# Kernel tuning notes

Measured on AMD Instinct MI355X. Metric: run time of the kernel, lower is better.

Reference implementation:

```python
import jax, jax.numpy as jnp
import numpy as np

N = 32768      # nodes
E = 262144     # edges (avg degree 8)
D = 128        # d_model (= per-head out_channels, concat=False)
H = 4          # heads
C = D          # out_channels per head
R = 64         # rel_dim (edge_dim)
NREL = 64      # n_rels
L = 2          # num_layers
LEAK = 0.2     # GATv2 leaky_relu slope
LN_EPS = 1e-5


def setup_inputs() -> dict:
    key = jax.random.key(0)
    ks = jax.random.split(key, 12)
    sdD = 1.0 / np.sqrt(D)
    sdR = 1.0 / np.sqrt(R)
    return {
        "x_flat": jax.random.normal(ks[0], (N, D), jnp.float32),
        "edge_index": jax.random.randint(ks[1], (2, E), 0, N, jnp.int64),
        "edge_type": jax.random.randint(ks[2], (E,), 0, NREL, jnp.int64),
        "valid_mask_flat": jnp.ones((N,), bool),
        "rel_emb": jax.random.normal(ks[3], (NREL, R), jnp.float32) * 0.1,
        "Wl": jax.random.normal(ks[4], (L, D, H * C), jnp.float32) * sdD,
        "bl": jnp.zeros((L, H * C), jnp.float32),
        "Wr": jax.random.normal(ks[5], (L, D, H * C), jnp.float32) * sdD,
        "br": jnp.zeros((L, H * C), jnp.float32),
        "We": jax.random.normal(ks[6], (L, R, H * C), jnp.float32) * sdR,
        "att": jax.random.normal(ks[7], (L, H, C), jnp.float32) * 0.1,
        "bias_o": jnp.zeros((L, D), jnp.float32),
        "ln_g": jnp.ones((L, D), jnp.float32),
        "ln_b": jnp.zeros((L, D), jnp.float32),
    }


def _gatv2_layer(h, src, dst, ea, Wl, bl, Wr, br, We, att, b):
    # h: [N,D]; src/dst: [E+N]; ea: [E+N,R] edge embeddings (incl. self loops)
    xl = (h @ Wl + bl).reshape(N, H, C)   # source transform
    xr = (h @ Wr + br).reshape(N, H, C)   # target transform
    ep = (ea @ We).reshape(-1, H, C)
    e = jax.nn.leaky_relu(xl[src] + xr[dst] + ep, LEAK)   # [E+N,H,C]
    logits = jnp.einsum('ehc,hc->eh', e, att)             # [E+N,H]
    # segment softmax over destination node
    m = jax.ops.segment_max(logits, dst, num_segments=N)
    m = jnp.where(jnp.isfinite(m), m, 0.0)
    p = jnp.exp(logits - m[dst])
    denom = jax.ops.segment_sum(p, dst, num_segments=N)
    alpha = p / (denom[dst] + 1e-16)                      # [E+N,H]
    out = jax.ops.segment_sum(alpha[:, :, None] * xl[src], dst, num_segments=N)
    return out.mean(axis=1) + b                           # concat=False -> head mean


def reference(x_flat, edge_index, edge_type, valid_mask_flat,
              rel_emb, Wl, bl, Wr, br, We, att, bias_o, ln_g, ln_b):
    x = jnp.where(valid_mask_flat[:, None], x_flat, 0.0)
    src, dst = edge_index[0], edge_index[1]
    ea = rel_emb[edge_type]                               # [E,R]
    # PyG add_self_loops with fill_value='mean': self-loop edge_attr is the
    # mean of incoming edge attrs per target node (0 if no incoming edges).
    ones = jnp.ones((E,), x.dtype)
    deg = jax.ops.segment_sum(ones, dst, num_segments=N)
    self_attr = jax.ops.segment_sum(ea, dst, num_segments=N) / jnp.maximum(deg, 1.0)[:, None]
    loop = jnp.arange(N, dtype=src.dtype)
    src_f = jnp.concatenate([src, loop])
    dst_f = jnp.concatenate([dst, loop])
    ea_f = jnp.concatenate([ea, self_attr], axis=0)

    h = x
    for l in range(L):
        msg = _gatv2_layer(h, src_f, dst_f, ea_f,
                           Wl[l], bl[l], Wr[l], br[l], We[l], att[l], bias_o[l])
        msg = jax.nn.gelu(msg, approximate=False)         # dropout = identity (eval)
        hn = h + msg
        mu = jnp.mean(hn, axis=-1, keepdims=True)
        var = jnp.mean(jnp.square(hn - mu), axis=-1, keepdims=True)
        h = (hn - mu) / jnp.sqrt(var + LN_EPS) * ln_g[l] + ln_b[l]
    return jnp.where(valid_mask_flat[:, None], h, 0.0)
```

## Files before the change

### kernel.cpp

```cpp
#include <hip/hip_runtime.h>
#include <hip/hip_bf16.h>
#include <math.h>

#define NN 32768
#define EE 262144
#define DM 128
#define HH 4
#define CC 128
#define HC 512
#define RD 64
#define NRELS 64
#define LEAKS 0.2f
#define LNEPS 1e-5f

typedef __hip_bfloat16 bf16;
typedef __attribute__((ext_vector_type(8))) short short8;
typedef __attribute__((ext_vector_type(4))) float f32x4;

__device__ __forceinline__ void unpack8(uint4 u, float* f) {
    f[0] = __uint_as_float((u.x & 0xffffu) << 16);
    f[1] = __uint_as_float(u.x & 0xffff0000u);
    f[2] = __uint_as_float((u.y & 0xffffu) << 16);
    f[3] = __uint_as_float(u.y & 0xffff0000u);
    f[4] = __uint_as_float((u.z & 0xffffu) << 16);
    f[5] = __uint_as_float(u.z & 0xffff0000u);
    f[6] = __uint_as_float((u.w & 0xffffu) << 16);
    f[7] = __uint_as_float(u.w & 0xffff0000u);
}

__global__ void k_deg(const int* __restrict__ dst, int* __restrict__ deg) {
    int e = blockIdx.x * 256 + threadIdx.x;
    if (e < EE) atomicAdd(&deg[dst[e]], 1);
}

__global__ void k_scan1(const int* __restrict__ deg, int* __restrict__ rowptr,
                        int* __restrict__ bsum) {
    __shared__ int s[256];
    int b = blockIdx.x, t = threadIdx.x;
    int v = deg[b * 256 + t];
    s[t] = v;
    __syncthreads();
    for (int off = 1; off < 256; off <<= 1) {
        int x = (t >= off) ? s[t - off] : 0;
        __syncthreads();
        s[t] += x;
        __syncthreads();
    }
    rowptr[b * 256 + t] = s[t] - v;
    if (t == 255) bsum[b] = s[255];
}

__global__ void k_scan2(const int* __restrict__ bsum, int* __restrict__ boff) {
    __shared__ int s[128];
    int t = threadIdx.x;
    int v = bsum[t];
    s[t] = v;
    __syncthreads();
    for (int off = 1; off < 128; off <<= 1) {
        int x = (t >= off) ? s[t - off] : 0;
        __syncthreads();
        s[t] += x;
        __syncthreads();
    }
    boff[t] = s[t] - v;
    if (t == 127) boff[128] = s[127];
}

__global__ void k_scan3(int* __restrict__ rowptr, const int* __restrict__ boff) {
    int i = blockIdx.x * 256 + threadIdx.x;
    rowptr[i] += boff[i >> 8];
    if (i == NN - 1) rowptr[NN] = boff[128];
}

__global__ void k_fill(const int* __restrict__ src, const int* __restrict__ dst,
                       const int* __restrict__ etype, const int* __restrict__ rowptr,
                       int* __restrict__ cursor, unsigned* __restrict__ csr) {
    int e = blockIdx.x * 256 + threadIdx.x;
    if (e < EE) {
        int d = dst[e];
        int pos = atomicAdd(&cursor[d], 1);
        csr[rowptr[d] + pos] = (unsigned)src[e] | ((unsigned)etype[e] << 16);
    }
}

__global__ void k_cast(const float* __restrict__ x, bf16* __restrict__ hb) {
    int i = blockIdx.x * 256 + threadIdx.x;
    const float4* p = (const float4*)x;
    float4 f0 = p[i * 2], f1 = p[i * 2 + 1];
    bf16 o[8];
    o[0] = __float2bfloat16(f0.x); o[1] = __float2bfloat16(f0.y);
    o[2] = __float2bfloat16(f0.z); o[3] = __float2bfloat16(f0.w);
    o[4] = __float2bfloat16(f1.x); o[5] = __float2bfloat16(f1.y);
    o[6] = __float2bfloat16(f1.z); o[7] = __float2bfloat16(f1.w);
    *reinterpret_cast<uint4*>(hb + (size_t)i * 8) = *reinterpret_cast<uint4*>(o);
}

__global__ void k_repack2(const float* __restrict__ Wl, const float* __restrict__ Wr,
                          bf16* __restrict__ Wt) {
    int idx = blockIdx.x * 256 + threadIdx.x;
    int l = idx >> 17;
    int rem = idx & 131071;
    int k = rem >> 10;
    int c = rem & 1023;
    const float* WlL = Wl + (size_t)l * DM * HC;
    const float* WrL = Wr + (size_t)l * DM * HC;
    float v = (c < HC) ? WlL[k * HC + c] : WrL[k * HC + (c - HC)];
    Wt[(size_t)l * 1024 * DM + (size_t)c * DM + k] = __float2bfloat16(v);
}

__global__ void k_wep2(const float* __restrict__ rel_emb, const float* __restrict__ We,
                       bf16* __restrict__ wep) {
    int l = blockIdx.x >> 6;
    int r = blockIdx.x & 63;
    int c = threadIdx.x;
    const float* WeL = We + (size_t)l * RD * HC;
    __shared__ float a[RD];
    if (c < RD) a[c] = rel_emb[r * RD + c];
    __syncthreads();
    float s = 0.f;
#pragma unroll 8
    for (int k = 0; k < RD; ++k) s += a[k] * WeL[k * HC + c];
    wep[(size_t)l * NRELS * HC + (size_t)r * HC + c] = __float2bfloat16(s);
}

__global__ __launch_bounds__(256) void k_gemm_mfma(
    const bf16* __restrict__ hb, const bf16* __restrict__ Wt,
    const float* __restrict__ bl, const float* __restrict__ br,
    bf16* __restrict__ xlb, bf16* __restrict__ xrb) {
    int lane = threadIdx.x & 63;
    int wave = threadIdx.x >> 6;
    int rbase = blockIdx.x * 32;
    int cbase = blockIdx.y * 256 + wave * 64;
    int lr = lane & 15;
    int lk = lane >> 4;
    const short* ha = (const short*)hb;
    const short* wa = (const short*)Wt;

    short8 a[2][4], b[4][4];
#pragma unroll
    for (int mi = 0; mi < 2; ++mi)
#pragma unroll
        for (int kk = 0; kk < 4; ++kk)
            a[mi][kk] = *(const short8*)(ha + (size_t)(rbase + mi * 16 + lr) * DM + kk * 32 + lk * 8);
#pragma unroll
    for (int ni = 0; ni < 4; ++ni)
#pragma unroll
        for (int kk = 0; kk < 4; ++kk)
            b[ni][kk] = *(const short8*)(wa + (size_t)(cbase + ni * 16 + lr) * DM + kk * 32 + lk * 8);

    f32x4 c[2][4];
#pragma unroll
    for (int mi = 0; mi < 2; ++mi)
#pragma unroll
        for (int ni = 0; ni < 4; ++ni)
            c[mi][ni] = (f32x4){0.f, 0.f, 0.f, 0.f};

#pragma unroll
    for (int kk = 0; kk < 4; ++kk)
#pragma unroll
        for (int mi = 0; mi < 2; ++mi)
#pragma unroll
            for (int ni = 0; ni < 4; ++ni)
                c[mi][ni] = __builtin_amdgcn_mfma_f32_16x16x32_bf16(
                    a[mi][kk], b[ni][kk], c[mi][ni], 0, 0, 0);

#pragma unroll
    for (int ni = 0; ni < 4; ++ni) {
        int col = cbase + ni * 16 + lr;
        float bv = (col < HC) ? bl[col] : br[col - HC];
        bf16* outp;
        int cc;
        if (col < HC) { outp = xlb; cc = col; } else { outp = xrb; cc = col - HC; }
#pragma unroll
        for (int mi = 0; mi < 2; ++mi) {
#pragma unroll
            for (int r = 0; r < 4; ++r) {
                int row = rbase + mi * 16 + lk * 4 + r;
                outp[(size_t)row * HC + cc] = __float2bfloat16(c[mi][ni][r] + bv);
            }
        }
    }
}

__global__ __launch_bounds__(1024, 8) void k_node(
    const bf16* __restrict__ xlb, const bf16* __restrict__ xrb,
    const bf16* __restrict__ wep,
    const unsigned* __restrict__ csr, const int* __restrict__ rowptr,
    const float* __restrict__ attL, const float* __restrict__ biasL,
    const float* __restrict__ lngL, const float* __restrict__ lnbL,
    const float* __restrict__ h_in, float* __restrict__ h_out,
    bf16* __restrict__ hb_out) {
    __shared__ short wepS[NRELS * HC];
    int tid = threadIdx.x;
    {
        const uint4* ws = (const uint4*)wep;
        uint4* wd = (uint4*)wepS;
#pragma unroll
        for (int i = 0; i < 4; ++i) wd[tid + i * 1024] = ws[tid + i * 1024];
    }
    __syncthreads();

    int lane = tid & 63;
    int wave = tid >> 6;
    int n = blockIdx.x * 16 + wave;
    int head = lane >> 4;
    const int g0 = lane * 8;
    const int ch0 = (lane & 15) * 8;
    const short* xla = (const short*)xlb;

    float attv[8];
#pragma unroll
    for (int j = 0; j < 8; ++j) attv[j] = attL[head * CC + ch0 + j];

    float xrn[8], xln[8];
    unpack8(*(const uint4*)((const short*)xrb + (size_t)n * HC + g0), xrn);
    unpack8(*(const uint4*)(xla + (size_t)n * HC + g0), xln);

    float m = -1e30f;
    float denom = 0.f;
    float acc[8], wpsum[8];
#pragma unroll
    for (int j = 0; j < 8; ++j) { acc[j] = 0.f; wpsum[j] = 0.f; }

    int r0 = rowptr[n], r1 = rowptr[n + 1];
    int d = r1 - r0;
    if (d > 0) {
        unsigned u = csr[r0];
        uint4 xv = *(const uint4*)(xla + (size_t)(u & 0xffffu) * HC + g0);
        for (int i = r0; i < r1; ++i) {
            int inx = (i + 1 < r1) ? (i + 1) : i;
            unsigned un = csr[inx];
            uint4 xn = *(const uint4*)(xla + (size_t)(un & 0xffffu) * HC + g0);
            uint4 wv = *(const uint4*)(wepS + (u >> 16) * HC + g0);
            float xs[8], wp[8];
            unpack8(xv, xs);
            unpack8(wv, wp);
            float p2 = 0.f;
#pragma unroll
            for (int j = 0; j < 8; ++j) {
                wpsum[j] += wp[j];
                float v = xs[j] + xrn[j] + wp[j];
                v = (v > 0.f) ? v : LEAKS * v;
                p2 += v * attv[j];
            }
            p2 += __shfl_xor(p2, 1);
            p2 += __shfl_xor(p2, 2);
            p2 += __shfl_xor(p2, 4);
            p2 += __shfl_xor(p2, 8);
            float mnew = fmaxf(m, p2);
            float scale = __expf(m - mnew);
            float p = __expf(p2 - mnew);
            denom = denom * scale + p;
#pragma unroll
            for (int j = 0; j < 8; ++j) acc[j] = acc[j] * scale + p * xs[j];
            m = mnew;
            u = un;
            xv = xn;
        }
    }

    float invd = (d > 0) ? (1.0f / (float)d) : 1.0f;
    float p2 = 0.f;
#pragma unroll
    for (int j = 0; j < 8; ++j) {
        float v = xln[j] + xrn[j] + wpsum[j] * invd;
        v = (v > 0.f) ? v : LEAKS * v;
        p2 += v * attv[j];
    }
    p2 += __shfl_xor(p2, 1);
    p2 += __shfl_xor(p2, 2);
    p2 += __shfl_xor(p2, 4);
    p2 += __shfl_xor(p2, 8);
    {
        float mnew = fmaxf(m, p2);
        float scale = __expf(m - mnew);
        float p = __expf(p2 - mnew);
        denom = denom * scale + p;
#pragma unroll
        for (int j = 0; j < 8; ++j) acc[j] = acc[j] * scale + p * xln[j];
    }

    float inv = 1.0f / (denom + 1e-16f);
    const float4* hp = (const float4*)(h_in + (size_t)n * DM + ch0);
    float4 h0 = hp[0], h1 = hp[1];
    float hin[8] = {h0.x, h0.y, h0.z, h0.w, h1.x, h1.y, h1.z, h1.w};
    float hn[8];
    float lsum = 0.f, lsq = 0.f;
#pragma unroll
    for (int j = 0; j < 8; ++j) {
        float v = acc[j] * inv;
        v += __shfl_xor(v, 16);
        v += __shfl_xor(v, 32);
        float x = v * 0.25f + biasL[ch0 + j];
        float ge = 0.5f * x * (1.0f + erff(x * 0.70710678f));
        float hv = hin[j] + ge;
        hn[j] = hv;
        lsum += hv;
        lsq += hv * hv;
    }
    lsum += __shfl_xor(lsum, 1);
    lsum += __shfl_xor(lsum, 2);
    lsum += __shfl_xor(lsum, 4);
    lsum += __shfl_xor(lsum, 8);
    lsq += __shfl_xor(lsq, 1);
    lsq += __shfl_xor(lsq, 2);
    lsq += __shfl_xor(lsq, 4);
    lsq += __shfl_xor(lsq, 8);
    float mu = lsum * (1.0f / 128.f);
    float var = lsq * (1.0f / 128.f) - mu * mu;
    float rstd = rsqrtf(var + LNEPS);
    if (lane < 16) {
#pragma unroll
        for (int j = 0; j < 8; ++j) {
            float o = (hn[j] - mu) * rstd * lngL[ch0 + j] + lnbL[ch0 + j];
            h_out[(size_t)n * DM + ch0 + j] = o;
            hb_out[(size_t)n * DM + ch0 + j] = __float2bfloat16(o);
        }
    }
}

extern "C" void kernel_launch(void* const* d_in, const int* in_sizes, int n_in,
                              void* d_out, int out_size, void* d_ws, size_t ws_size,
                              hipStream_t stream) {
    const float* x_flat   = (const float*)d_in[0];
    const int*   edge_idx = (const int*)d_in[1];
    const int*   edge_typ = (const int*)d_in[2];
    const float* rel_emb  = (const float*)d_in[4];
    const float* Wl       = (const float*)d_in[5];
    const float* bl       = (const float*)d_in[6];
    const float* Wr       = (const float*)d_in[7];
    const float* br       = (const float*)d_in[8];
    const float* We       = (const float*)d_in[9];
    const float* att      = (const float*)d_in[10];
    const float* bias_o   = (const float*)d_in[11];
    const float* ln_g     = (const float*)d_in[12];
    const float* ln_b     = (const float*)d_in[13];

    const int* srcp = edge_idx;
    const int* dstp = edge_idx + EE;

    char* w = (char*)d_ws;
    auto alloc = [&](size_t bytes) -> void* {
        void* p = (void*)w;
        w += (bytes + 255) & ~(size_t)255;
        return p;
    };
    bf16*  xlb    = (bf16*)alloc((size_t)NN * HC * 2);
    bf16*  xrb    = (bf16*)alloc((size_t)NN * HC * 2);
    bf16*  hb     = (bf16*)alloc((size_t)NN * DM * 2);
    float* h_mid  = (float*)alloc((size_t)NN * DM * 4);
    bf16*  wep    = (bf16*)alloc((size_t)2 * NRELS * HC * 2);
    bf16*  Wt     = (bf16*)alloc((size_t)2 * 1024 * DM * 2);
    int*   deg    = (int*)alloc((size_t)NN * 4);
    int*   rowptr = (int*)alloc((size_t)(NN + 1) * 4);
    int*   cursor = (int*)alloc((size_t)NN * 4);
    int*   bsum   = (int*)alloc((size_t)128 * 4);
    int*   boff   = (int*)alloc((size_t)129 * 4);
    unsigned* csr = (unsigned*)alloc((size_t)EE * 4);

    hipMemsetAsync(deg, 0, (size_t)NN * 4, stream);
    hipMemsetAsync(cursor, 0, (size_t)NN * 4, stream);

    k_deg<<<EE / 256, 256, 0, stream>>>(dstp, deg);
    k_scan1<<<NN / 256, 256, 0, stream>>>(deg, rowptr, bsum);
    k_scan2<<<1, 128, 0, stream>>>(bsum, boff);
    k_scan3<<<NN / 256, 256, 0, stream>>>(rowptr, boff);
    k_fill<<<EE / 256, 256, 0, stream>>>(srcp, dstp, edge_typ, rowptr, cursor, csr);
    k_cast<<<NN * DM / 8 / 256, 256, 0, stream>>>(x_flat, hb);
    k_wep2<<<128, 512, 0, stream>>>(rel_emb, We, wep);
    k_repack2<<<1024, 256, 0, stream>>>(Wl, Wr, Wt);

    const float* h = x_flat;
    for (int l = 0; l < 2; ++l) {
        k_gemm_mfma<<<dim3(NN / 32, 4), 256, 0, stream>>>(
            hb, Wt + (size_t)l * 1024 * DM,
            bl + (size_t)l * HC, br + (size_t)l * HC, xlb, xrb);
        float* hout = (l == 0) ? h_mid : (float*)d_out;
        k_node<<<NN / 16, 1024, 0, stream>>>(xlb, xrb, wep + (size_t)l * NRELS * HC,
                                             csr, rowptr,
                                             att + (size_t)l * HH * CC,
                                             bias_o + (size_t)l * DM,
                                             ln_g + (size_t)l * DM,
                                             ln_b + (size_t)l * DM,
                                             h, hout, hb);
        h = hout;
    }
}
```

Baseline: 462.1 us.

## Pair-unroll node aggregation, drop LDS staging, merge prep kernels

The node kernel now works through edges two at a time with prefetch of the next pair. It reads relation projections straight from global/L2 instead of staging 64KB into LDS per block, and it uses 256-thread blocks. The online softmax skips the rescale when no lane's max increases. Separately, the cast, repack and rel-projection kernels are merged into one launch, the two memsets are combined, edge kernels use 1024-thread blocks, and the final layer no longer writes an unused bf16 copy. The aim is to cut LDS fill overhead, launch count and latency-bound edge loop stalls, with the risk of more global gather traffic for the wep rows.

```diff
diff --git a/kernel.cpp b/kernel.cpp
--- a/kernel.cpp
+++ b/kernel.cpp
@@ -29,8 +29,8 @@
 }
 
 __global__ void k_deg(const int* __restrict__ dst, int* __restrict__ deg) {
-    int e = blockIdx.x * 256 + threadIdx.x;
-    if (e < EE) atomicAdd(&deg[dst[e]], 1);
+    int e = blockIdx.x * 1024 + threadIdx.x;
+    atomicAdd(&deg[dst[e]], 1);
 }
 
 __global__ void k_scan1(const int* __restrict__ deg, int* __restrict__ rowptr,
@@ -75,52 +75,52 @@
 __global__ void k_fill(const int* __restrict__ src, const int* __restrict__ dst,
                        const int* __restrict__ etype, const int* __restrict__ rowptr,
                        int* __restrict__ cursor, unsigned* __restrict__ csr) {
-    int e = blockIdx.x * 256 + threadIdx.x;
-    if (e < EE) {
-        int d = dst[e];
-        int pos = atomicAdd(&cursor[d], 1);
-        csr[rowptr[d] + pos] = (unsigned)src[e] | ((unsigned)etype[e] << 16);
-    }
-}
-
-__global__ void k_cast(const float* __restrict__ x, bf16* __restrict__ hb) {
-    int i = blockIdx.x * 256 + threadIdx.x;
-    const float4* p = (const float4*)x;
-    float4 f0 = p[i * 2], f1 = p[i * 2 + 1];
-    bf16 o[8];
-    o[0] = __float2bfloat16(f0.x); o[1] = __float2bfloat16(f0.y);
-    o[2] = __float2bfloat16(f0.z); o[3] = __float2bfloat16(f0.w);
-    o[4] = __float2bfloat16(f1.x); o[5] = __float2bfloat16(f1.y);
-    o[6] = __float2bfloat16(f1.z); o[7] = __float2bfloat16(f1.w);
-    *reinterpret_cast<uint4*>(hb + (size_t)i * 8) = *reinterpret_cast<uint4*>(o);
-}
-
-__global__ void k_repack2(const float* __restrict__ Wl, const float* __restrict__ Wr,
-                          bf16* __restrict__ Wt) {
-    int idx = blockIdx.x * 256 + threadIdx.x;
-    int l = idx >> 17;
-    int rem = idx & 131071;
-    int k = rem >> 10;
-    int c = rem & 1023;
-    const float* WlL = Wl + (size_t)l * DM * HC;
-    const float* WrL = Wr + (size_t)l * DM * HC;
-    float v = (c < HC) ? WlL[k * HC + c] : WrL[k * HC + (c - HC)];
-    Wt[(size_t)l * 1024 * DM + (size_t)c * DM + k] = __float2bfloat16(v);
-}
-
-__global__ void k_wep2(const float* __restrict__ rel_emb, const float* __restrict__ We,
+    int e = blockIdx.x * 1024 + threadIdx.x;
+    int d = dst[e];
+    int pos = atomicAdd(&cursor[d], 1);
+    csr[rowptr[d] + pos] = (unsigned)src[e] | ((unsigned)etype[e] << 16);
+}
+
+__global__ void k_prep(const float* __restrict__ x, bf16* __restrict__ hb,
+                       const float* __restrict__ Wl, const float* __restrict__ Wr,
+                       bf16* __restrict__ Wt,
+                       const float* __restrict__ rel_emb, const float* __restrict__ We,
                        bf16* __restrict__ wep) {
-    int l = blockIdx.x >> 6;
-    int r = blockIdx.x & 63;
-    int c = threadIdx.x;
-    const float* WeL = We + (size_t)l * RD * HC;
-    __shared__ float a[RD];
-    if (c < RD) a[c] = rel_emb[r * RD + c];
-    __syncthreads();
-    float s = 0.f;
+    __shared__ float sa[RD];
+    int b = blockIdx.x, tid = threadIdx.x;
+    if (b < 2048) {
+        int i = b * 256 + tid;
+        const float4* p = (const float4*)x;
+        float4 f0 = p[i * 2], f1 = p[i * 2 + 1];
+        bf16 o[8];
+        o[0] = __float2bfloat16(f0.x); o[1] = __float2bfloat16(f0.y);
+        o[2] = __float2bfloat16(f0.z); o[3] = __float2bfloat16(f0.w);
+        o[4] = __float2bfloat16(f1.x); o[5] = __float2bfloat16(f1.y);
+        o[6] = __float2bfloat16(f1.z); o[7] = __float2bfloat16(f1.w);
+        *reinterpret_cast<uint4*>(hb + (size_t)i * 8) = *reinterpret_cast<uint4*>(o);
+    } else if (b < 3072) {
+        int idx = (b - 2048) * 256 + tid;
+        int l = idx >> 17;
+        int rem = idx & 131071;
+        int k = rem >> 10;
+        int c = rem & 1023;
+        const float* WlL = Wl + (size_t)l * DM * HC;
+        const float* WrL = Wr + (size_t)l * DM * HC;
+        float v = (c < HC) ? WlL[k * HC + c] : WrL[k * HC + (c - HC)];
+        Wt[(size_t)l * 1024 * DM + (size_t)c * DM + k] = __float2bfloat16(v);
+    } else {
+        int blk = b - 3072;
+        int l = blk >> 6, r = blk & 63;
+        const float* WeL = We + (size_t)l * RD * HC;
+        if (tid < RD) sa[tid] = rel_emb[r * RD + tid];
+        __syncthreads();
+        for (int c = tid; c < HC; c += 256) {
+            float s = 0.f;
 #pragma unroll 8
-    for (int k = 0; k < RD; ++k) s += a[k] * WeL[k * HC + c];
-    wep[(size_t)l * NRELS * HC + (size_t)r * HC + c] = __float2bfloat16(s);
+            for (int k = 0; k < RD; ++k) s += sa[k] * WeL[k * HC + c];
+            wep[(size_t)l * NRELS * HC + (size_t)r * HC + c] = __float2bfloat16(s);
+        }
+    }
 }
 
 __global__ __launch_bounds__(256) void k_gemm_mfma(
@@ -182,7 +182,7 @@
     }
 }
 
-__global__ __launch_bounds__(1024, 8) void k_node(
+__global__ __launch_bounds__(256, 5) void k_node(
     const bf16* __restrict__ xlb, const bf16* __restrict__ xrb,
     const bf16* __restrict__ wep,
     const unsigned* __restrict__ csr, const int* __restrict__ rowptr,
@@ -190,31 +190,22 @@
     const float* __restrict__ lngL, const float* __restrict__ lnbL,
     const float* __restrict__ h_in, float* __restrict__ h_out,
     bf16* __restrict__ hb_out) {
-    __shared__ short wepS[NRELS * HC];
     int tid = threadIdx.x;
-    {
-        const uint4* ws = (const uint4*)wep;
-        uint4* wd = (uint4*)wepS;
-#pragma unroll
-        for (int i = 0; i < 4; ++i) wd[tid + i * 1024] = ws[tid + i * 1024];
-    }
-    __syncthreads();
-
     int lane = tid & 63;
     int wave = tid >> 6;
-    int n = blockIdx.x * 16 + wave;
+    int n = blockIdx.x * 4 + wave;
     int head = lane >> 4;
     const int g0 = lane * 8;
     const int ch0 = (lane & 15) * 8;
     const short* xla = (const short*)xlb;
+    const short* wpa_base = (const short*)wep;
 
     float attv[8];
 #pragma unroll
     for (int j = 0; j < 8; ++j) attv[j] = attL[head * CC + ch0 + j];
 
-    float xrn[8], xln[8];
+    float xrn[8];
     unpack8(*(const uint4*)((const short*)xrb + (size_t)n * HC + g0), xrn);
-    unpack8(*(const uint4*)(xla + (size_t)n * HC + g0), xln);
 
     float m = -1e30f;
     float denom = 0.f;
@@ -224,41 +215,109 @@
 
     int r0 = rowptr[n], r1 = rowptr[n + 1];
     int d = r1 - r0;
-    if (d > 0) {
-        unsigned u = csr[r0];
+    int npair = d >> 1;
+    const unsigned* cp = csr + r0;
+
+    unsigned ua = 0, ub = 0;
+    uint4 xva, xvb, wva, wvb;
+    if (npair > 0) {
+        ua = cp[0]; ub = cp[1];
+        xva = *(const uint4*)(xla + (size_t)(ua & 0xffffu) * HC + g0);
+        xvb = *(const uint4*)(xla + (size_t)(ub & 0xffffu) * HC + g0);
+        wva = *(const uint4*)(wpa_base + (size_t)(ua >> 16) * HC + g0);
+        wvb = *(const uint4*)(wpa_base + (size_t)(ub >> 16) * HC + g0);
+    }
+    for (int p = 0; p < npair; ++p) {
+        int i2 = p * 2 + 2;
+        int ia = (i2 < d) ? i2 : (d - 1);
+        int ib = (i2 + 1 < d) ? (i2 + 1) : (d - 1);
+        unsigned una = cp[ia], unb = cp[ib];
+        uint4 xna = *(const uint4*)(xla + (size_t)(una & 0xffffu) * HC + g0);
+        uint4 xnb = *(const uint4*)(xla + (size_t)(unb & 0xffffu) * HC + g0);
+        uint4 wna = *(const uint4*)(wpa_base + (size_t)(una >> 16) * HC + g0);
+        uint4 wnb = *(const uint4*)(wpa_base + (size_t)(unb >> 16) * HC + g0);
+
+        float xsa[8], xsb[8], wa[8], wb[8];
+        unpack8(xva, xsa);
+        unpack8(xvb, xsb);
+        unpack8(wva, wa);
+        unpack8(wvb, wb);
+        float p2a = 0.f, p2b = 0.f;
+#pragma unroll
+        for (int j = 0; j < 8; ++j) {
+            wpsum[j] += wa[j] + wb[j];
+            float va = xsa[j] + xrn[j] + wa[j];
+            va = (va > 0.f) ? va : LEAKS * va;
+            p2a += va * attv[j];
+            float vb = xsb[j] + xrn[j] + wb[j];
+            vb = (vb > 0.f) ? vb : LEAKS * vb;
+            p2b += vb * attv[j];
+        }
+        p2a += __shfl_xor(p2a, 1); p2b += __shfl_xor(p2b, 1);
+        p2a += __shfl_xor(p2a, 2); p2b += __shfl_xor(p2b, 2);
+        p2a += __shfl_xor(p2a, 4); p2b += __shfl_xor(p2b, 4);
+        p2a += __shfl_xor(p2a, 8); p2b += __shfl_xor(p2b, 8);
+
+        float pmax = fmaxf(p2a, p2b);
+        if (__any(pmax > m)) {
+            float mnew = fmaxf(m, pmax);
+            float scale = __expf(m - mnew);
+            float pa = __expf(p2a - mnew);
+            float pb = __expf(p2b - mnew);
+            denom = denom * scale + pa + pb;
+#pragma unroll
+            for (int j = 0; j < 8; ++j)
+                acc[j] = acc[j] * scale + pa * xsa[j] + pb * xsb[j];
+            m = mnew;
+        } else {
+            float pa = __expf(p2a - m);
+            float pb = __expf(p2b - m);
+            denom += pa + pb;
+#pragma unroll
+            for (int j = 0; j < 8; ++j)
+                acc[j] += pa * xsa[j] + pb * xsb[j];
+        }
+        ua = una; ub = unb;
+        xva = xna; xvb = xnb;
+        wva = wna; wvb = wnb;
+    }
+    if (d & 1) {
+        unsigned u = cp[d - 1];
         uint4 xv = *(const uint4*)(xla + (size_t)(u & 0xffffu) * HC + g0);
-        for (int i = r0; i < r1; ++i) {
-            int inx = (i + 1 < r1) ? (i + 1) : i;
-            unsigned un = csr[inx];
-            uint4 xn = *(const uint4*)(xla + (size_t)(un & 0xffffu) * HC + g0);
-            uint4 wv = *(const uint4*)(wepS + (u >> 16) * HC + g0);
-            float xs[8], wp[8];
-            unpack8(xv, xs);
-            unpack8(wv, wp);
-            float p2 = 0.f;
-#pragma unroll
-            for (int j = 0; j < 8; ++j) {
-                wpsum[j] += wp[j];
-                float v = xs[j] + xrn[j] + wp[j];
-                v = (v > 0.f) ? v : LEAKS * v;
-                p2 += v * attv[j];
-            }
-            p2 += __shfl_xor(p2, 1);
-            p2 += __shfl_xor(p2, 2);
-            p2 += __shfl_xor(p2, 4);
-            p2 += __shfl_xor(p2, 8);
+        uint4 wv = *(const uint4*)(wpa_base + (size_t)(u >> 16) * HC + g0);
+        float xs[8], wp[8];
+        unpack8(xv, xs);
+        unpack8(wv, wp);
+        float p2 = 0.f;
+#pragma unroll
+        for (int j = 0; j < 8; ++j) {
+            wpsum[j] += wp[j];
+            float v = xs[j] + xrn[j] + wp[j];
+            v = (v > 0.f) ? v : LEAKS * v;
+            p2 += v * attv[j];
+        }
+        p2 += __shfl_xor(p2, 1);
+        p2 += __shfl_xor(p2, 2);
+        p2 += __shfl_xor(p2, 4);
+        p2 += __shfl_xor(p2, 8);
+        if (__any(p2 > m)) {
             float mnew = fmaxf(m, p2);
             float scale = __expf(m - mnew);
-            float p = __expf(p2 - mnew);
-            denom = denom * scale + p;
-#pragma unroll
-            for (int j = 0; j < 8; ++j) acc[j] = acc[j] * scale + p * xs[j];
+            float pe = __expf(p2 - mnew);
+            denom = denom * scale + pe;
+#pragma unroll
+            for (int j = 0; j < 8; ++j) acc[j] = acc[j] * scale + pe * xs[j];
             m = mnew;
-            u = un;
-            xv = xn;
-        }
-    }
-
+        } else {
+            float pe = __expf(p2 - m);
+            denom += pe;
+#pragma unroll
+            for (int j = 0; j < 8; ++j) acc[j] += pe * xs[j];
+        }
+    }
+
+    float xln[8];
+    unpack8(*(const uint4*)(xla + (size_t)n * HC + g0), xln);
     float invd = (d > 0) ? (1.0f / (float)d) : 1.0f;
     float p2 = 0.f;
 #pragma unroll
@@ -274,10 +333,10 @@
     {
         float mnew = fmaxf(m, p2);
         float scale = __expf(m - mnew);
-        float p = __expf(p2 - mnew);
-        denom = denom * scale + p;
-#pragma unroll
-        for (int j = 0; j < 8; ++j) acc[j] = acc[j] * scale + p * xln[j];
+        float pe = __expf(p2 - mnew);
+        denom = denom * scale + pe;
+#pragma unroll
+        for (int j = 0; j < 8; ++j) acc[j] = acc[j] * scale + pe * xln[j];
     }
 
     float inv = 1.0f / (denom + 1e-16f);
@@ -314,7 +373,7 @@
         for (int j = 0; j < 8; ++j) {
             float o = (hn[j] - mu) * rstd * lngL[ch0 + j] + lnbL[ch0 + j];
             h_out[(size_t)n * DM + ch0 + j] = o;
-            hb_out[(size_t)n * DM + ch0 + j] = __float2bfloat16(o);
+            if (hb_out) hb_out[(size_t)n * DM + ch0 + j] = __float2bfloat16(o);
         }
     }
 }
@@ -352,23 +411,20 @@
     bf16*  wep    = (bf16*)alloc((size_t)2 * NRELS * HC * 2);
     bf16*  Wt     = (bf16*)alloc((size_t)2 * 1024 * DM * 2);
     int*   deg    = (int*)alloc((size_t)NN * 4);
+    int*   cursor = (int*)alloc((size_t)NN * 4);
     int*   rowptr = (int*)alloc((size_t)(NN + 1) * 4);
-    int*   cursor = (int*)alloc((size_t)NN * 4);
     int*   bsum   = (int*)alloc((size_t)128 * 4);
     int*   boff   = (int*)alloc((size_t)129 * 4);
     unsigned* csr = (unsigned*)alloc((size_t)EE * 4);
 
-    hipMemsetAsync(deg, 0, (size_t)NN * 4, stream);
-    hipMemsetAsync(cursor, 0, (size_t)NN * 4, stream);
-
-    k_deg<<<EE / 256, 256, 0, stream>>>(dstp, deg);
+    hipMemsetAsync(deg, 0, (size_t)NN * 8, stream);
+
+    k_deg<<<EE / 1024, 1024, 0, stream>>>(dstp, deg);
     k_scan1<<<NN / 256, 256, 0, stream>>>(deg, rowptr, bsum);
     k_scan2<<<1, 128, 0, stream>>>(bsum, boff);
     k_scan3<<<NN / 256, 256, 0, stream>>>(rowptr, boff);
-    k_fill<<<EE / 256, 256, 0, stream>>>(srcp, dstp, edge_typ, rowptr, cursor, csr);
-    k_cast<<<NN * DM / 8 / 256, 256, 0, stream>>>(x_flat, hb);
-    k_wep2<<<128, 512, 0, stream>>>(rel_emb, We, wep);
-    k_repack2<<<1024, 256, 0, stream>>>(Wl, Wr, Wt);
+    k_fill<<<EE / 1024, 1024, 0, stream>>>(srcp, dstp, edge_typ, rowptr, cursor, csr);
+    k_prep<<<3200, 256, 0, stream>>>(x_flat, hb, Wl, Wr, Wt, rel_emb, We, wep);
 
     const float* h = x_flat;
     for (int l = 0; l < 2; ++l) {
@@ -376,13 +432,13 @@
             hb, Wt + (size_t)l * 1024 * DM,
             bl + (size_t)l * HC, br + (size_t)l * HC, xlb, xrb);
         float* hout = (l == 0) ? h_mid : (float*)d_out;
-        k_node<<<NN / 16, 1024, 0, stream>>>(xlb, xrb, wep + (size_t)l * NRELS * HC,
-                                             csr, rowptr,
-                                             att + (size_t)l * HH * CC,
-                                             bias_o + (size_t)l * DM,
-                                             ln_g + (size_t)l * DM,
-                                             ln_b + (size_t)l * DM,
-                                             h, hout, hb);
+        k_node<<<NN / 4, 256, 0, stream>>>(xlb, xrb, wep + (size_t)l * NRELS * HC,
+                                           csr, rowptr,
+                                           att + (size_t)l * HH * CC,
+                                           bias_o + (size_t)l * DM,
+                                           ln_g + (size_t)l * DM,
+                                           ln_b + (size_t)l * DM,
+                                           h, hout, (l == 0) ? hb : (bf16*)nullptr);
         h = hout;
     }
 }
```

Measured after the change: 658.2 us. 1.42x slower.
